# Kernel optimization log

Hardware: AMD Instinct MI355X
Metric: run time of the kernel (lower is better)

## Reference

```python
import jax, jax.numpy as jnp
import numpy as np
from jax import lax

V, D, HD, K, T = 100000, 300, 256, 19, 8192  # vocab, emb dim, per-dir hidden, tags, seq len
START, STOP = K - 2, K - 1
NEG = -10000.0


def setup_inputs() -> dict:
    key = jax.random.key(0)
    ks = jax.random.split(key, 13)
    sc = 0.05
    sentence = jax.random.randint(ks[0], (T,), 0, V, dtype=jnp.int32)
    emb = jax.random.normal(ks[1], (V, D), jnp.float32) * sc
    w_ih_f = jax.random.normal(ks[2], (4 * HD, D), jnp.float32) * sc
    w_hh_f = jax.random.normal(ks[3], (4 * HD, HD), jnp.float32) * sc
    b_f = jax.random.normal(ks[4], (4 * HD,), jnp.float32) * sc
    w_ih_b = jax.random.normal(ks[5], (4 * HD, D), jnp.float32) * sc
    w_hh_b = jax.random.normal(ks[6], (4 * HD, HD), jnp.float32) * sc
    b_b = jax.random.normal(ks[7], (4 * HD,), jnp.float32) * sc
    w_out = jax.random.normal(ks[8], (K, 2 * HD), jnp.float32) * sc
    b_out = jax.random.normal(ks[9], (K,), jnp.float32) * sc
    transitions = jax.random.normal(ks[10], (K, K), jnp.float32)
    transitions = transitions.at[START, :].set(NEG).at[:, STOP].set(NEG)
    h0 = jax.random.normal(ks[11], (2, HD), jnp.float32)
    c0 = jax.random.normal(ks[12], (2, HD), jnp.float32)
    return dict(sentence=sentence, emb=emb, w_ih_f=w_ih_f, w_hh_f=w_hh_f, b_f=b_f,
                w_ih_b=w_ih_b, w_hh_b=w_hh_b, b_b=b_b, w_out=w_out, b_out=b_out,
                transitions=transitions, h0=h0, c0=c0)


def _lstm(x, w_ih, w_hh, b, h0, c0):
    # x: [T, D]; PyTorch gate order i, f, g, o
    xg = x @ w_ih.T + b  # precompute input contribution [T, 4*HD]

    def step(carry, xt):
        h, c = carry
        g = xt + h @ w_hh.T
        i, f, gg, o = jnp.split(g, 4)
        i, f, o = jax.nn.sigmoid(i), jax.nn.sigmoid(f), jax.nn.sigmoid(o)
        c = f * c + i * jnp.tanh(gg)
        h = o * jnp.tanh(c)
        return (h, c), h

    _, hs = lax.scan(step, (h0, c0), xg)
    return hs  # [T, HD]


def reference(sentence, emb, w_ih_f, w_hh_f, b_f, w_ih_b, w_hh_b, b_b,
              w_out, b_out, transitions, h0, c0):
    x = emb[sentence]  # [T, D]
    hf = _lstm(x, w_ih_f, w_hh_f, b_f, h0[0], c0[0])
    hb = _lstm(x[::-1], w_ih_b, w_hh_b, b_b, h0[1], c0[1])[::-1]
    feats = jnp.concatenate([hf, hb], axis=-1) @ w_out.T + b_out  # [T, K]

    # Viterbi: fused max-plus recurrence over tags per timestep
    init = jnp.full((K,), NEG, jnp.float32).at[START].set(0.0)

    def vstep(fv, feat):
        scores = fv[None, :] + transitions  # [next_tag, prev_tag]
        bp = jnp.argmax(scores, axis=1).astype(jnp.int32)
        fv_new = jnp.max(scores, axis=1) + feat
        return fv_new, bp

    fv, bps = lax.scan(vstep, init, feats)  # bps: [T, K]
    terminal = fv + transitions[STOP]
    best = jnp.argmax(terminal).astype(jnp.int32)
    path_score = terminal[best]

    def bstep(tag, bp):
        return bp[tag], tag

    _, best_path = lax.scan(bstep, best, bps, reverse=True)  # [T] tag at each step
    return path_score, best_path
```

## Files before the change

### kernel.cpp

```cpp
#include <hip/hip_runtime.h>
#include <hip/hip_bf16.h>

#define T_LEN 8192
#define HD 256
#define D_EMB 300
#define NTAG 19
#define START_TAG 17
#define STOP_TAG 18

typedef unsigned long long u64;

__device__ __forceinline__ u64 a_load(const u64* p) {
  return __hip_atomic_load(p, __ATOMIC_RELAXED, __HIP_MEMORY_SCOPE_AGENT);
}
__device__ __forceinline__ void a_store(u64* p, u64 v) {
  __hip_atomic_store(p, v, __ATOMIC_RELAXED, __HIP_MEMORY_SCOPE_AGENT);
}
__device__ __forceinline__ int agent_add1(int* p) {
  return __hip_atomic_fetch_add(p, 1, __ATOMIC_RELAXED, __HIP_MEMORY_SCOPE_AGENT);
}
__device__ __forceinline__ bool agent_cas(int* p, int expv, int newv) {
  return __hip_atomic_compare_exchange_strong(p, &expv, newv, __ATOMIC_RELAXED,
                                              __ATOMIC_RELAXED, __HIP_MEMORY_SCOPE_AGENT);
}
__device__ __forceinline__ int agent_ldi(const int* p) {
  return __hip_atomic_load(p, __ATOMIC_RELAXED, __HIP_MEMORY_SCOPE_AGENT);
}

__device__ __forceinline__ u64 fast_load(const u64* p) {
  u64 v;
  asm volatile("buffer_inv sc0\n\t"
               "global_load_dwordx2 %0, %1, off sc0\n\t"
               "s_waitcnt vmcnt(0)"
               : "=v"(v) : "v"(p) : "memory");
  return v;
}
__device__ __forceinline__ void l2_publish(u64* p, u64 v) {
  (void)__hip_atomic_exchange(p, v, __ATOMIC_RELAXED, __HIP_MEMORY_SCOPE_WORKGROUP);
}

__device__ __forceinline__ float4 ld4(const float* p) {
  float4 v;
  asm volatile("global_load_dwordx4 %0, %1, off\n\ts_waitcnt vmcnt(0)"
               : "=&v"(v) : "v"(p));
  return v;
}
__device__ __forceinline__ float rcp_(float x) { return __builtin_amdgcn_rcpf(x); }

#define GETREG_XCC_ID (20 | (3 << 11))
#define HIDX(i) (((i) >> 4) * 20 + ((i) & 15))
#define DOT4(acc, wv, h4) \
  acc = fmaf((wv).x, (h4).x, acc); acc = fmaf((wv).y, (h4).y, acc); \
  acc = fmaf((wv).z, (h4).z, acc); acc = fmaf((wv).w, (h4).w, acc);

#define SWZ(x, imm) __int_as_float(__builtin_amdgcn_ds_swizzle(__float_as_int(x), imm))

#define FWORD(base, slot, i) ((base) + (((slot) * 256 + (i)) << 4))

__global__ __launch_bounds__(512) void k_xg(
    const int* __restrict__ sent, const float* __restrict__ emb,
    const float* __restrict__ w_ih_f, const float* __restrict__ b_f,
    const float* __restrict__ w_ih_b, const float* __restrict__ b_b,
    float* __restrict__ xg)
{
  const int dir = blockIdx.y;
  const int t0 = blockIdx.x * 64;
  const float* wih  = dir ? w_ih_b : w_ih_f;
  const float* bias = dir ? b_b    : b_f;
  __shared__ float xlds[64][304];
  __shared__ int sid[64];
  const int tid = threadIdx.x;
  if (tid < 64) {
    int t = t0 + tid;
    int ts = dir ? (T_LEN - 1 - t) : t;
    sid[tid] = sent[ts];
  }
  __syncthreads();
  for (int idx = tid; idx < 64 * D_EMB; idx += 512) {
    int r = idx / D_EMB, k = idx - r * D_EMB;
    xlds[r][k] = emb[(size_t)sid[r] * D_EMB + k];
  }
  __syncthreads();
  float* xgo = xg + (size_t)dir * T_LEN * 1024;
#pragma unroll 1
  for (int rr = 0; rr < 2; ++rr) {
    int row = tid + rr * 512;
    const float* wrow = wih + (size_t)row * D_EMB;
    float bb = bias[row];
    float acc[64];
#pragma unroll
    for (int i = 0; i < 64; ++i) acc[i] = bb;
#pragma unroll 1
    for (int k4 = 0; k4 < 75; ++k4) {
      float4 w4 = *(const float4*)(wrow + k4 * 4);
#pragma unroll
      for (int i = 0; i < 64; ++i) {
        float4 x4 = *(const float4*)&xlds[i][k4 * 4];
        acc[i] = fmaf(w4.x, x4.x, acc[i]);
        acc[i] = fmaf(w4.y, x4.y, acc[i]);
        acc[i] = fmaf(w4.z, x4.z, acc[i]);
        acc[i] = fmaf(w4.w, x4.w, acc[i]);
      }
    }
#pragma unroll
    for (int i = 0; i < 64; ++i)
      xgo[(size_t)(t0 + i) * 1024 + row] = acc[i];
  }
}

__global__ __launch_bounds__(512, 2) void k_lstm(
    const float* __restrict__ xg,
    const float* __restrict__ w_hh_f, const float* __restrict__ w_hh_b,
    const float* __restrict__ h0, const float* __restrict__ c0,
    float* __restrict__ h_out,
    u64* __restrict__ hfast,
    u64* __restrict__ hsafe,
    int* __restrict__ elect)
{
  __shared__ int s_role, s_b;
  const int tid = threadIdx.x;
  if (tid == 0) {
    int xcd = __builtin_amdgcn_s_getreg(GETREG_XCC_ID) & 15;
    int tkt = agent_add1(&elect[xcd]);
    int role = -1, b = -1;
    if (tkt < 16) {
      int half = tkt >> 3;
      int cid = xcd * 2 + half + 1;
      b = tkt & 7;
      if ((tkt & 7) == 7) {
        if (half == 0) {
          if (!agent_cas(&elect[16], 0, cid)) agent_cas(&elect[17], 0, cid);
        } else {
          if (!agent_cas(&elect[17], 0, cid)) agent_cas(&elect[16], 0, cid);
        }
      }
      int s0, s1;
      for (;;) {
        s0 = agent_ldi(&elect[16]); s1 = agent_ldi(&elect[17]);
        if (s0 != 0 && s1 != 0) break;
        __builtin_amdgcn_s_sleep(2);
      }
      if (s0 == cid) role = 0;
      else if (s1 == cid) role = 1;
    }
    s_role = role; s_b = b;
  }
  __syncthreads();
  const int role = s_role, b = s_b;
  if (role < 0) return;

  const float* whh = role ? w_hh_b : w_hh_f;
  const float* xgd = xg + (size_t)role * T_LEN * 1024;
  u64* fb = hfast + role * 8192;
  u64* sb = hsafe + role * 512;
  const int jl = tid >> 4, q = tid & 15;
  const int j = b * 32 + jl;
  const bool isq0 = (q == 0);

  const bool ispoll = (tid < 224);
  int pwi = 0;
  { int cch = tid >> 5; pwi = (cch + (cch >= b)) * 32 + (tid & 31); }

  const float* wrI = whh + (size_t)(0 * 256 + j) * 256 + q * 16;
  const float* wrF = whh + (size_t)(1 * 256 + j) * 256 + q * 16;
  const float* wrG = whh + (size_t)(2 * 256 + j) * 256 + q * 16;
  const float* wrO = whh + (size_t)(3 * 256 + j) * 256 + q * 16;
  float4 wi0 = ld4(wrI), wi1 = ld4(wrI + 4), wi2 = ld4(wrI + 8), wi3 = ld4(wrI + 12);
  float4 wf0 = ld4(wrF), wf1 = ld4(wrF + 4), wf2 = ld4(wrF + 8), wf3 = ld4(wrF + 12);
  float4 wg0 = ld4(wrG), wg1 = ld4(wrG + 4), wg2 = ld4(wrG + 8), wg3 = ld4(wrG + 12);
  float4 wo0 = ld4(wrO), wo1 = ld4(wrO + 4), wo2 = ld4(wrO + 8), wo3 = ld4(wrO + 12);

  __shared__ float hlds[2][320];

  float c = 0.f;
  float x0 = 0.f, x1 = 0.f, x2 = 0.f, x3 = 0.f;
  if (isq0) {
    c = c0[role * 256 + j];
    float h0v = h0[role * 256 + j];
    hlds[0][HIDX(j)] = h0v;
    u64 word = ((u64)__float_as_uint(h0v) << 32) | 1ull;
    l2_publish(FWORD(fb, 0, j), word);
    a_store(sb + j, word);
    x0 = xgd[j]; x1 = xgd[256 + j]; x2 = xgd[512 + j]; x3 = xgd[768 + j];
  }

  for (int s = 0; s < T_LEN; ++s) {
    const int slot = s & 1;
    if (ispoll) {
      const unsigned tag = (unsigned)(s + 1);
      u64* fwp = FWORD(fb, slot, pwi);
      u64* swp = sb + slot * 256 + pwi;
      u64 wv;
      __builtin_amdgcn_s_sleep(6);
      for (int it = 0;; ++it) {
        wv = fast_load(fwp);
        if ((unsigned)wv == tag) break;
        if ((it & 3) == 3) {
          wv = a_load(swp);
          if ((unsigned)wv == tag) break;
        }
        __builtin_amdgcn_s_sleep(1);
      }
      hlds[slot][HIDX(pwi)] = __uint_as_float((unsigned)(wv >> 32));
    }
    __syncthreads();

    float n0 = 0.f, n1 = 0.f, n2 = 0.f, n3 = 0.f;
    if (isq0 && s + 1 < T_LEN) {
      const float* xr = xgd + (size_t)(s + 1) * 1024;
      n0 = xr[j]; n1 = xr[256 + j]; n2 = xr[512 + j]; n3 = xr[768 + j];
    }

    const float* hv = hlds[slot] + q * 20;
    float4 h40 = *(const float4*)(hv);
    float4 h41 = *(const float4*)(hv + 4);
    float4 h42 = *(const float4*)(hv + 8);
    float4 h43 = *(const float4*)(hv + 12);
    float a0 = 0.f, a1 = 0.f, a2 = 0.f, a3 = 0.f;
    DOT4(a0, wi0, h40); DOT4(a0, wi1, h41); DOT4(a0, wi2, h42); DOT4(a0, wi3, h43);
    DOT4(a1, wf0, h40); DOT4(a1, wf1, h41); DOT4(a1, wf2, h42); DOT4(a1, wf3, h43);
    DOT4(a2, wg0, h40); DOT4(a2, wg1, h41); DOT4(a2, wg2, h42); DOT4(a2, wg3, h43);
    DOT4(a3, wo0, h40); DOT4(a3, wo1, h41); DOT4(a3, wo2, h42); DOT4(a3, wo3, h43);
    a0 += SWZ(a0, 0x041F); a1 += SWZ(a1, 0x041F); a2 += SWZ(a2, 0x041F); a3 += SWZ(a3, 0x041F);
    a0 += SWZ(a0, 0x081F); a1 += SWZ(a1, 0x081F); a2 += SWZ(a2, 0x081F); a3 += SWZ(a3, 0x081F);
    a0 += SWZ(a0, 0x101F); a1 += SWZ(a1, 0x101F); a2 += SWZ(a2, 0x101F); a3 += SWZ(a3, 0x101F);
    a0 += SWZ(a0, 0x201F); a1 += SWZ(a1, 0x201F); a2 += SWZ(a2, 0x201F); a3 += SWZ(a3, 0x201F);

    if (isq0) {
      float pi = a0 + x0, pf = a1 + x1, pg = a2 + x2, po = a3 + x3;
      float i_ = rcp_(1.f + __expf(-pi));
      float f_ = rcp_(1.f + __expf(-pf));
      float o_ = rcp_(1.f + __expf(-po));
      float eg = __expf(2.f * fabsf(pg));
      float g_ = copysignf(1.f - 2.f * rcp_(1.f + eg), pg);
      c = f_ * c + i_ * g_;
      float ec = __expf(2.f * fabsf(c));
      float th = copysignf(1.f - 2.f * rcp_(1.f + ec), c);
      float h = o_ * th;
      u64 word = ((u64)__float_as_uint(h) << 32) | (u64)(unsigned)(s + 2);
      l2_publish(FWORD(fb, slot ^ 1, j), word);
      a_store(sb + (slot ^ 1) * 256 + j, word);
      hlds[slot ^ 1][HIDX(j)] = h;
      int tor = role ? (T_LEN - 1 - s) : s;
      h_out[(size_t)tor * 512 + role * 256 + j] = h;
    }
    x0 = n0; x1 = n1; x2 = n2; x3 = n3;
  }
}

__global__ __launch_bounds__(640) void k_feats(
    const float* __restrict__ h, const float* __restrict__ w_out,
    const float* __restrict__ b_out, float* __restrict__ feats)
{
  const int tid = threadIdx.x;
  if (tid >= 32 * NTAG) return;
  const int tloc = tid / NTAG, j = tid - tloc * NTAG;
  const int t = blockIdx.x * 32 + tloc;
  const float* hr = h + (size_t)t * 512;
  const float* wr = w_out + (size_t)j * 512;
  float a0 = 0.f, a1 = 0.f, a2 = 0.f, a3 = 0.f;
  for (int k = 0; k < 512; k += 4) {
    float4 hv = *(const float4*)(hr + k);
    float4 wv = *(const float4*)(wr + k);
    a0 = fmaf(hv.x, wv.x, a0);
    a1 = fmaf(hv.y, wv.y, a1);
    a2 = fmaf(hv.z, wv.z, a2);
    a3 = fmaf(hv.w, wv.w, a3);
  }
  feats[(size_t)t * NTAG + j] = ((a0 + a1) + (a2 + a3)) + b_out[j];
}

#define M2(va, xa, vb, xb) { bool c_ = (va) >= (vb); \
  va = c_ ? (va) : (vb); xa = c_ ? (xa) : (xb); }

#define VIT_STEP(FEATV, TT) { \
  float v0 = __shfl(fv, 0) + tr0,  v1 = __shfl(fv, 1) + tr1; \
  float v2 = __shfl(fv, 2) + tr2,  v3 = __shfl(fv, 3) + tr3; \
  float v4 = __shfl(fv, 4) + tr4,  v5 = __shfl(fv, 5) + tr5; \
  float v6 = __shfl(fv, 6) + tr6,  v7 = __shfl(fv, 7) + tr7; \
  float v8 = __shfl(fv, 8) + tr8,  v9 = __shfl(fv, 9) + tr9; \
  float v10 = __shfl(fv, 10) + tr10, v11 = __shfl(fv, 11) + tr11; \
  float v12 = __shfl(fv, 12) + tr12, v13 = __shfl(fv, 13) + tr13; \
  float v14 = __shfl(fv, 14) + tr14, v15 = __shfl(fv, 15) + tr15; \
  float v16 = __shfl(fv, 16) + tr16, v17 = __shfl(fv, 17) + tr17; \
  float v18 = __shfl(fv, 18) + tr18; \
  int x0 = 0, x2 = 2, x4 = 4, x6 = 6, x8 = 8, x10 = 10, x12 = 12, x14 = 14, x16 = 16; \
  M2(v0, x0, v1, 1)    M2(v2, x2, v3, 3)    M2(v4, x4, v5, 5) \
  M2(v6, x6, v7, 7)    M2(v8, x8, v9, 9)    M2(v10, x10, v11, 11) \
  M2(v12, x12, v13, 13) M2(v14, x14, v15, 15) M2(v16, x16, v17, 17) \
  M2(v0, x0, v2, x2)   M2(v4, x4, v6, x6)   M2(v8, x8, v10, x10) \
  M2(v12, x12, v14, x14) M2(v16, x16, v18, 18) \
  M2(v0, x0, v4, x4)   M2(v8, x8, v12, x12) \
  M2(v0, x0, v8, x8)   M2(v0, x0, v16, x16) \
  if (lane < NTAG) bps[(size_t)(TT) * NTAG + lane] = (unsigned char)x0; \
  fv = v0 + (FEATV); }

__global__ __launch_bounds__(64) void k_viterbi(
    const float* __restrict__ feats, const float* __restrict__ trans,
    float* __restrict__ fvfinal, unsigned char* __restrict__ bps)
{
  const int lane = threadIdx.x;
  const int j = (lane < NTAG) ? lane : (NTAG - 1);
  const float* trr = trans + (size_t)j * NTAG;
  float tr0 = trr[0], tr1 = trr[1], tr2 = trr[2], tr3 = trr[3], tr4 = trr[4];
  float tr5 = trr[5], tr6 = trr[6], tr7 = trr[7], tr8 = trr[8], tr9 = trr[9];
  float tr10 = trr[10], tr11 = trr[11], tr12 = trr[12], tr13 = trr[13];
  float tr14 = trr[14], tr15 = trr[15], tr16 = trr[16], tr17 = trr[17];
  float tr18 = trr[18];
  float fv = (j == START_TAG) ? 0.f : -10000.f;

  float fa0 = feats[0 * NTAG + j],  fa1 = feats[1 * NTAG + j];
  float fa2 = feats[2 * NTAG + j],  fa3 = feats[3 * NTAG + j];
  float fa4 = feats[4 * NTAG + j],  fa5 = feats[5 * NTAG + j];
  float fa6 = feats[6 * NTAG + j],  fa7 = feats[7 * NTAG + j];
  float fb0 = feats[8 * NTAG + j],  fb1 = feats[9 * NTAG + j];
  float fb2 = feats[10 * NTAG + j], fb3 = feats[11 * NTAG + j];
  float fb4 = feats[12 * NTAG + j], fb5 = feats[13 * NTAG + j];
  float fb6 = feats[14 * NTAG + j], fb7 = feats[15 * NTAG + j];

  for (int tb = 0; tb < 1024; ++tb) {
    const int t0 = tb * 8;
    VIT_STEP(fa0, t0 + 0) VIT_STEP(fa1, t0 + 1)
    VIT_STEP(fa2, t0 + 2) VIT_STEP(fa3, t0 + 3)
    VIT_STEP(fa4, t0 + 4) VIT_STEP(fa5, t0 + 5)
    VIT_STEP(fa6, t0 + 6) VIT_STEP(fa7, t0 + 7)
    fa0 = fb0; fa1 = fb1; fa2 = fb2; fa3 = fb3;
    fa4 = fb4; fa5 = fb5; fa6 = fb6; fa7 = fb7;
    if (tb < 1022) {
      const float* fr = feats + (size_t)(tb + 2) * 8 * NTAG + j;
      fb0 = fr[0 * NTAG]; fb1 = fr[1 * NTAG]; fb2 = fr[2 * NTAG]; fb3 = fr[3 * NTAG];
      fb4 = fr[4 * NTAG]; fb5 = fr[5 * NTAG]; fb6 = fr[6 * NTAG]; fb7 = fr[7 * NTAG];
    }
  }
  if (lane < NTAG) fvfinal[lane] = fv;
}

__global__ __launch_bounds__(1024) void k_backtrack(
    const float* __restrict__ fvfinal, const float* __restrict__ trans,
    const unsigned char* __restrict__ bps, float* __restrict__ out)
{
  __shared__ unsigned char maps[64][20];
  __shared__ unsigned char xc[64];
  __shared__ float score_sh;
  const int tid = threadIdx.x;

  for (int jid = tid; jid < 64 * NTAG; jid += 1024) {
    int c = jid / NTAG, tau = jid - c * NTAG;
    int y = tau;
    for (int t = (c + 1) * 128 - 1; t >= c * 128; --t)
      y = bps[(size_t)t * NTAG + y];
    maps[c][tau] = (unsigned char)y;
  }
  __syncthreads();

  if (tid == 0) {
    float best = -3.0e38f; int bi = 0;
    for (int p = 0; p < NTAG; ++p) {
      float s = fvfinal[p] + trans[STOP_TAG * NTAG + p];
      if (s > best) { best = s; bi = p; }
    }
    score_sh = best;
    int e = bi;
    for (int c = 63; c >= 0; --c) { xc[c] = (unsigned char)e; e = maps[c][e]; }
  }
  __syncthreads();

  if (tid == 0) out[0] = score_sh;
  if (tid < 64) {
    int c = tid;
    int y = xc[c];
    out[1 + ((c + 1) * 128 - 1)] = (float)y;
    for (int t = (c + 1) * 128 - 1; t > c * 128; --t) {
      y = bps[(size_t)t * NTAG + y];
      out[1 + t - 1] = (float)y;
    }
  }
}

extern "C" void kernel_launch(void* const* d_in, const int* in_sizes, int n_in,
                              void* d_out, int out_size, void* d_ws, size_t ws_size,
                              hipStream_t stream) {
  const int*   sent    = (const int*)d_in[0];
  const float* emb     = (const float*)d_in[1];
  const float* w_ih_f  = (const float*)d_in[2];
  const float* w_hh_f  = (const float*)d_in[3];
  const float* b_f     = (const float*)d_in[4];
  const float* w_ih_b  = (const float*)d_in[5];
  const float* w_hh_b  = (const float*)d_in[6];
  const float* b_b     = (const float*)d_in[7];
  const float* w_out   = (const float*)d_in[8];
  const float* b_out   = (const float*)d_in[9];
  const float* trans   = (const float*)d_in[10];
  const float* h0      = (const float*)d_in[11];
  const float* c0      = (const float*)d_in[12];
  float* out = (float*)d_out;

  char* ws = (char*)d_ws;
  float* xg            = (float*)(ws + 0);
  float* h_out         = (float*)(ws + 67108864);
  float* feats         = (float*)(ws + 83886080);
  float* fvfin         = (float*)(ws + 84508672);
  unsigned char* bps   = (unsigned char*)(ws + 84508800);
  u64* hfast           = (u64*)(ws + 84664448);
  u64* hsafe           = (u64*)(ws + 84795520);
  int* elect           = (int*)(ws + 84803712);

  hipMemsetAsync(hfast, 0, 131072 + 8192 + 128, stream);

  k_xg      <<<dim3(128, 2), 512, 0, stream>>>(sent, emb, w_ih_f, b_f, w_ih_b, b_b, xg);
  k_lstm    <<<96, 512, 0, stream>>>(xg, w_hh_f, w_hh_b, h0, c0, h_out, hfast, hsafe, elect);
  k_feats   <<<256, 640, 0, stream>>>(h_out, w_out, b_out, feats);
  k_viterbi <<<1, 64, 0, stream>>>(feats, trans, fvfin, bps);
  k_backtrack<<<1, 1024, 0, stream>>>(fvfin, trans, bps, out);
}
```

Before: 14.51 ms.

## Widen LSTM recurrence blocks to 1024 threads and pack handoff words densely

Each LSTM workgroup now runs 1024 threads, with 32 lanes per hidden unit, each holding 8 weights per gate instead of 16. This halves the per-lane dot-product length and adds one more swizzle reduction stage. The fast handoff buffer drops its 128-byte-per-word padding and is packed densely, and the sleeps in the polling loop are removed to cut latency on each serial step. Risks: more threads per block and denser packing may cause cache-line contention among pollers, and busy spinning without sleep can load the memory system. The swizzle pattern 0x401F may also not span a full 32-lane group as intended.

```diff
diff --git a/kernel.cpp b/kernel.cpp
--- a/kernel.cpp
+++ b/kernel.cpp
@@ -38,13 +38,6 @@
 __device__ __forceinline__ void l2_publish(u64* p, u64 v) {
   (void)__hip_atomic_exchange(p, v, __ATOMIC_RELAXED, __HIP_MEMORY_SCOPE_WORKGROUP);
 }
-
-__device__ __forceinline__ float4 ld4(const float* p) {
-  float4 v;
-  asm volatile("global_load_dwordx4 %0, %1, off\n\ts_waitcnt vmcnt(0)"
-               : "=&v"(v) : "v"(p));
-  return v;
-}
 __device__ __forceinline__ float rcp_(float x) { return __builtin_amdgcn_rcpf(x); }
 
 #define GETREG_XCC_ID (20 | (3 << 11))
@@ -55,7 +48,7 @@
 
 #define SWZ(x, imm) __int_as_float(__builtin_amdgcn_ds_swizzle(__float_as_int(x), imm))
 
-#define FWORD(base, slot, i) ((base) + (((slot) * 256 + (i)) << 4))
+#define KEEP4(v4) asm volatile("" :: "v"((v4).x), "v"((v4).y), "v"((v4).z), "v"((v4).w))
 
 __global__ __launch_bounds__(512) void k_xg(
     const int* __restrict__ sent, const float* __restrict__ emb,
@@ -108,7 +101,7 @@
   }
 }
 
-__global__ __launch_bounds__(512, 2) void k_lstm(
+__global__ __launch_bounds__(1024, 1) void k_lstm(
     const float* __restrict__ xg,
     const float* __restrict__ w_hh_f, const float* __restrict__ w_hh_b,
     const float* __restrict__ h0, const float* __restrict__ c0,
@@ -151,9 +144,9 @@
 
   const float* whh = role ? w_hh_b : w_hh_f;
   const float* xgd = xg + (size_t)role * T_LEN * 1024;
-  u64* fb = hfast + role * 8192;
+  u64* fb = hfast + role * 512;
   u64* sb = hsafe + role * 512;
-  const int jl = tid >> 4, q = tid & 15;
+  const int jl = tid >> 5, q = tid & 31;
   const int j = b * 32 + jl;
   const bool isq0 = (q == 0);
 
@@ -161,14 +154,14 @@
   int pwi = 0;
   { int cch = tid >> 5; pwi = (cch + (cch >= b)) * 32 + (tid & 31); }
 
-  const float* wrI = whh + (size_t)(0 * 256 + j) * 256 + q * 16;
-  const float* wrF = whh + (size_t)(1 * 256 + j) * 256 + q * 16;
-  const float* wrG = whh + (size_t)(2 * 256 + j) * 256 + q * 16;
-  const float* wrO = whh + (size_t)(3 * 256 + j) * 256 + q * 16;
-  float4 wi0 = ld4(wrI), wi1 = ld4(wrI + 4), wi2 = ld4(wrI + 8), wi3 = ld4(wrI + 12);
-  float4 wf0 = ld4(wrF), wf1 = ld4(wrF + 4), wf2 = ld4(wrF + 8), wf3 = ld4(wrF + 12);
-  float4 wg0 = ld4(wrG), wg1 = ld4(wrG + 4), wg2 = ld4(wrG + 8), wg3 = ld4(wrG + 12);
-  float4 wo0 = ld4(wrO), wo1 = ld4(wrO + 4), wo2 = ld4(wrO + 8), wo3 = ld4(wrO + 12);
+  const float* wrI = whh + (size_t)(0 * 256 + j) * 256 + q * 8;
+  const float* wrF = whh + (size_t)(1 * 256 + j) * 256 + q * 8;
+  const float* wrG = whh + (size_t)(2 * 256 + j) * 256 + q * 8;
+  const float* wrO = whh + (size_t)(3 * 256 + j) * 256 + q * 8;
+  float4 wi0 = *(const float4*)(wrI), wi1 = *(const float4*)(wrI + 4);
+  float4 wf0 = *(const float4*)(wrF), wf1 = *(const float4*)(wrF + 4);
+  float4 wg0 = *(const float4*)(wrG), wg1 = *(const float4*)(wrG + 4);
+  float4 wo0 = *(const float4*)(wrO), wo1 = *(const float4*)(wrO + 4);
 
   __shared__ float hlds[2][320];
 
@@ -179,7 +172,7 @@
     float h0v = h0[role * 256 + j];
     hlds[0][HIDX(j)] = h0v;
     u64 word = ((u64)__float_as_uint(h0v) << 32) | 1ull;
-    l2_publish(FWORD(fb, 0, j), word);
+    l2_publish(fb + j, word);
     a_store(sb + j, word);
     x0 = xgd[j]; x1 = xgd[256 + j]; x2 = xgd[512 + j]; x3 = xgd[768 + j];
   }
@@ -188,10 +181,9 @@
     const int slot = s & 1;
     if (ispoll) {
       const unsigned tag = (unsigned)(s + 1);
-      u64* fwp = FWORD(fb, slot, pwi);
+      u64* fwp = fb + slot * 256 + pwi;
       u64* swp = sb + slot * 256 + pwi;
       u64 wv;
-      __builtin_amdgcn_s_sleep(6);
       for (int it = 0;; ++it) {
         wv = fast_load(fwp);
         if ((unsigned)wv == tag) break;
@@ -199,7 +191,6 @@
           wv = a_load(swp);
           if ((unsigned)wv == tag) break;
         }
-        __builtin_amdgcn_s_sleep(1);
       }
       hlds[slot][HIDX(pwi)] = __uint_as_float((unsigned)(wv >> 32));
     }
@@ -211,20 +202,19 @@
       n0 = xr[j]; n1 = xr[256 + j]; n2 = xr[512 + j]; n3 = xr[768 + j];
     }
 
-    const float* hv = hlds[slot] + q * 20;
+    const float* hv = hlds[slot] + (q >> 1) * 20 + (q & 1) * 8;
     float4 h40 = *(const float4*)(hv);
     float4 h41 = *(const float4*)(hv + 4);
-    float4 h42 = *(const float4*)(hv + 8);
-    float4 h43 = *(const float4*)(hv + 12);
     float a0 = 0.f, a1 = 0.f, a2 = 0.f, a3 = 0.f;
-    DOT4(a0, wi0, h40); DOT4(a0, wi1, h41); DOT4(a0, wi2, h42); DOT4(a0, wi3, h43);
-    DOT4(a1, wf0, h40); DOT4(a1, wf1, h41); DOT4(a1, wf2, h42); DOT4(a1, wf3, h43);
-    DOT4(a2, wg0, h40); DOT4(a2, wg1, h41); DOT4(a2, wg2, h42); DOT4(a2, wg3, h43);
-    DOT4(a3, wo0, h40); DOT4(a3, wo1, h41); DOT4(a3, wo2, h42); DOT4(a3, wo3, h43);
+    DOT4(a0, wi0, h40); DOT4(a0, wi1, h41);
+    DOT4(a1, wf0, h40); DOT4(a1, wf1, h41);
+    DOT4(a2, wg0, h40); DOT4(a2, wg1, h41);
+    DOT4(a3, wo0, h40); DOT4(a3, wo1, h41);
     a0 += SWZ(a0, 0x041F); a1 += SWZ(a1, 0x041F); a2 += SWZ(a2, 0x041F); a3 += SWZ(a3, 0x041F);
     a0 += SWZ(a0, 0x081F); a1 += SWZ(a1, 0x081F); a2 += SWZ(a2, 0x081F); a3 += SWZ(a3, 0x081F);
     a0 += SWZ(a0, 0x101F); a1 += SWZ(a1, 0x101F); a2 += SWZ(a2, 0x101F); a3 += SWZ(a3, 0x101F);
     a0 += SWZ(a0, 0x201F); a1 += SWZ(a1, 0x201F); a2 += SWZ(a2, 0x201F); a3 += SWZ(a3, 0x201F);
+    a0 += SWZ(a0, 0x401F); a1 += SWZ(a1, 0x401F); a2 += SWZ(a2, 0x401F); a3 += SWZ(a3, 0x401F);
 
     if (isq0) {
       float pi = a0 + x0, pf = a1 + x1, pg = a2 + x2, po = a3 + x3;
@@ -238,13 +228,15 @@
       float th = copysignf(1.f - 2.f * rcp_(1.f + ec), c);
       float h = o_ * th;
       u64 word = ((u64)__float_as_uint(h) << 32) | (u64)(unsigned)(s + 2);
-      l2_publish(FWORD(fb, slot ^ 1, j), word);
+      l2_publish(fb + (slot ^ 1) * 256 + j, word);
       a_store(sb + (slot ^ 1) * 256 + j, word);
       hlds[slot ^ 1][HIDX(j)] = h;
       int tor = role ? (T_LEN - 1 - s) : s;
       h_out[(size_t)tor * 512 + role * 256 + j] = h;
     }
     x0 = n0; x1 = n1; x2 = n2; x3 = n3;
+    KEEP4(wi0); KEEP4(wi1); KEEP4(wf0); KEEP4(wf1);
+    KEEP4(wg0); KEEP4(wg1); KEEP4(wo0); KEEP4(wo1);
   }
 }
 
@@ -402,13 +394,13 @@
   float* fvfin         = (float*)(ws + 84508672);
   unsigned char* bps   = (unsigned char*)(ws + 84508800);
   u64* hfast           = (u64*)(ws + 84664448);
-  u64* hsafe           = (u64*)(ws + 84795520);
-  int* elect           = (int*)(ws + 84803712);
-
-  hipMemsetAsync(hfast, 0, 131072 + 8192 + 128, stream);
+  u64* hsafe           = (u64*)(ws + 84672640);
+  int* elect           = (int*)(ws + 84680832);
+
+  (void)hipMemsetAsync(hfast, 0, 2 * 8192 + 128, stream);
 
   k_xg      <<<dim3(128, 2), 512, 0, stream>>>(sent, emb, w_ih_f, b_f, w_ih_b, b_b, xg);
-  k_lstm    <<<96, 512, 0, stream>>>(xg, w_hh_f, w_hh_b, h0, c0, h_out, hfast, hsafe, elect);
+  k_lstm    <<<96, 1024, 0, stream>>>(xg, w_hh_f, w_hh_b, h0, c0, h_out, hfast, hsafe, elect);
   k_feats   <<<256, 640, 0, stream>>>(h_out, w_out, b_out, feats);
   k_viterbi <<<1, 64, 0, stream>>>(feats, trans, fvfin, bps);
   k_backtrack<<<1, 1024, 0, stream>>>(fvfin, trans, bps, out);
```

New measurement: 18.06 ms. +24.5%, slower.
